# Kernel tuning notes

Hardware: AMD Instinct MI355X
Metric: run time of the kernel (lower is better)

The kernel has to match this reference:

```python
import jax, jax.numpy as jnp
import numpy as np

# ---- init_kwargs constants ----
OFFSET = 1.0
TAU = 10.0
HX, HY = 1.0, 1.0
B, C, NX0, NY0 = 8, 1, 384, 384
KMAX = 30          # forward() calls BiCGSTAB_GS(kmax=30)
EPS = 1e-9
# forward() transposes dims 2,3 and swaps nx,ny:
NX, NY = NY0, NX0


def sym_pad(x):
    # torchvision Pad(1, padding_mode='symmetric')
    return jnp.pad(x, ((0, 0), (0, 0), (1, 1), (1, 1)), mode='symmetric')


def zero_pad(x):
    return jnp.pad(x, ((0, 0), (0, 0), (1, 1), (1, 1)))


def zero_pad_gs(x):
    return zero_pad(x[:, :, 1:NX + 1, 1:NY + 1])


def fro(x):
    # Frobenius norm over spatial dims, NaN-safe at 0 for AD.
    sq = jnp.sum(x * x, axis=(2, 3))
    return jnp.where(sq > 0, jnp.sqrt(jnp.where(sq > 0, sq, 1.0)), 0.0)


def make_stencil(V, mask1, mask2):
    Vp = jnp.swapaxes(sym_pad(V), 2, 3) + OFFSET          # (B,C,NX+2,NY+2)
    m1 = jnp.swapaxes(sym_pad(mask1), 2, 3)
    m2 = jnp.swapaxes(sym_pad(mask2), 2, 3)
    # conv2d(V,f1)/conv2d(V,f2): forward-diff / pairwise average
    d1r = ((Vp[:, :, 1:, :] - Vp[:, :, :-1, :]) / HX) / (0.5 * (Vp[:, :, 1:, :] + Vp[:, :, :-1, :]))
    d2r = ((Vp[:, :, :, 1:] - Vp[:, :, :, :-1]) / HY) / (0.5 * (Vp[:, :, :, 1:] + Vp[:, :, :, :-1]))
    d1 = jnp.zeros((B, C, NX + 2, NY + 2), V.dtype).at[:, :, :NX + 1, 1:NY + 1].set(d1r[:, :, :, 1:NY + 1]) * m1
    d2 = jnp.zeros((B, C, NX + 2, NY + 2), V.dtype).at[:, :, 1:NX + 1, :NY + 1].set(d2r[:, :, 1:NX + 1, :]) * m2
    rx, ry = TAU / (2.0 * HX), TAU / (2.0 * HY)
    rxx, ryy = TAU / (HX * HX), TAU / (HY * HY)
    # conv 'same' with kernels [1,-1,0]: out[i] = d[i-1] - d[i] (zero beyond edge)
    dd1 = jnp.pad(d1, ((0, 0), (0, 0), (1, 0), (0, 0)))[:, :, :-1, :] - d1
    dd2 = jnp.pad(d2, ((0, 0), (0, 0), (0, 0), (1, 0)))[:, :, :, :-1] - d2
    boo = (1.0 + 2.0 * (rxx + ryy) - rx * dd1 - ry * dd2)[:, :, 1:NX + 1, 1:NY + 1]
    bpo = -rxx + rx * d1[:, :, 1:NX + 1, 1:NY + 1]
    bop = -ryy + ry * d2[:, :, 1:NX + 1, 1:NY + 1]
    bmo = -rxx - rx * d1[:, :, :NX, 1:NY + 1]
    bom = -ryy - ry * d2[:, :, 1:NX + 1, :NY]
    return boo, bmo, bom, bop, bpo


def apply_stencil(x, st):
    boo, bmo, bom, bop, bpo = st
    inp = sym_pad(x[:, :, 1:NX + 1, 1:NY + 1])
    res = (boo * inp[:, :, 1:NX + 1, 1:NY + 1]
           + bmo * inp[:, :, :NX, 1:NY + 1]
           + bom * inp[:, :, 1:NX + 1, :NY]
           + bop * inp[:, :, 1:NX + 1, 2:NY + 2]
           + bpo * inp[:, :, 2:NX + 2, 1:NY + 1])
    return zero_pad(res)


def bicgstab(x, b, st):
    thr = EPS * NX * NY
    r0 = apply_stencil(x, st)
    p = zero_pad_gs(b - r0)
    r_0, r = p, p
    r0_abs = fro(p)
    r_abs = r0_abs
    zs = jnp.zeros((B, C), x.dtype)
    k = jnp.zeros((B, C), jnp.int32)
    z4 = jnp.zeros_like(x)
    carry = (x, r_0, r, z4, p, z4, z4, z4, k, r_abs, zs, r0_abs, zs, zs, zs, zs)

    def step(c, _):
        x, r_0, r, r_old, p, v, s, t, k, r_abs, v_abs, r0_abs, sigma, alpha, omega, beta = c
        CONV = (k < KMAX) & (r_abs > thr)
        CONVe = CONV[:, :, None, None]
        v = jnp.where(CONVe, apply_stencil(p, st), v)
        sigma = jnp.where(CONV, jnp.sum(v * r_0, (2, 3)), sigma)
        v_abs = jnp.where(CONV, fro(v), v_abs)
        RES = sigma <= EPS * v_abs * r0_abs
        R1 = CONV & RES
        R1e = R1[:, :, None, None]
        p = jnp.where(R1e, zero_pad_gs(b - apply_stencil(x, st)), p)
        r = jnp.where(R1e, p, r)
        r_0 = jnp.where(R1e, p, r_0)
        r0_abs = jnp.where(R1, fro(r_0), r0_abs)
        r_abs = jnp.where(R1, r0_abs, r_abs)
        k = jnp.where(R1, k + 1, k)
        NR = CONV & ~RES
        NRe = NR[:, :, None, None]
        sig_safe = jnp.where(NR, sigma, 1.0)
        alpha = jnp.where(NR, jnp.sum(r * r_0, (2, 3)) / sig_safe, alpha)
        s = jnp.where(NRe, r - alpha[:, :, None, None] * v, s)
        C2 = fro(s) <= thr
        C3 = NR & C2
        C3e = C3[:, :, None, None]
        x = jnp.where(C3e, x + alpha[:, :, None, None] * p, x)
        r = jnp.where(C3e, s, r)
        C4 = NR & ~C2
        C4e = C4[:, :, None, None]
        t = jnp.where(C4e, apply_stencil(s, st), t)
        tt = jnp.where(C4, jnp.sum(t * t, (2, 3)), 1.0)
        omega = jnp.where(C4, jnp.sum(t * s, (2, 3)) / tt, omega)
        x = jnp.where(C4e, x + alpha[:, :, None, None] * p + omega[:, :, None, None] * s, x)
        r_old = jnp.where(C4e, r, r_old)
        r = jnp.where(C4e, s - omega[:, :, None, None] * t, r)
        om_safe = jnp.where(C4, omega, 1.0)
        den = jnp.where(C4, jnp.sum(r_old * r_0, (2, 3)), 1.0)
        beta = jnp.where(C4, alpha / om_safe * (jnp.sum(r * r_0, (2, 3)) / den), beta)
        p = jnp.where(C4e, r + beta[:, :, None, None] * (p - omega[:, :, None, None] * v), p)
        k = jnp.where(NR, k + 1, k)
        r_abs = jnp.where(NR, fro(r), r_abs)
        return (x, r_0, r, r_old, p, v, s, t, k, r_abs, v_abs, r0_abs, sigma, alpha, omega, beta), None

    carry, _ = jax.lax.scan(step, carry, None, length=KMAX)
    return carry[0]


def setup_inputs():
    key = jax.random.key(0)
    k1, k2, k3 = jax.random.split(key, 3)
    V = jax.random.uniform(k1, (B, C, NX0, NY0), jnp.float32)
    mask1 = jax.random.uniform(k2, (B, C, NX0, NY0), jnp.float32)
    mask2 = jax.random.uniform(k3, (B, C, NX0, NY0), jnp.float32)
    return {"V": V, "mask1": mask1, "mask2": mask2}


def reference(V, mask1, mask2):
    st = make_stencil(V, mask1, mask2)
    Um = jnp.mean(V, axis=(2, 3), keepdims=True) * jnp.ones_like(V)
    U = jnp.swapaxes(sym_pad(Um), 2, 3) + OFFSET
    x = bicgstab(U, U, st)   # BiCGSTAB_GS(x=U, b=U)
    return x[:, :, 1:-1, 1:-1]
```

## Files before the change

kernel.cpp:

```cpp
#include <hip/hip_runtime.h>

#define NXI 384
#define NG  (NXI*NXI)
#define NSYS 8
#define BPS 32
#define NBLK (NSYS*BPS)
#define NTHR 512
#define ROWS_PB 12
#define EPB (ROWS_PB*NXI)
#define EPT (EPB/NTHR)

#define THRC 1.47456e-4f

__device__ __forceinline__ float aloadf(const float* p) {
  return __hip_atomic_load(p, __ATOMIC_RELAXED, __HIP_MEMORY_SCOPE_AGENT);
}
__device__ __forceinline__ void astoref(float* p, float v) {
  __hip_atomic_store(p, v, __ATOMIC_RELAXED, __HIP_MEMORY_SCOPE_AGENT);
}
__device__ __forceinline__ double aloadd(const double* p) {
  return __hip_atomic_load(p, __ATOMIC_RELAXED, __HIP_MEMORY_SCOPE_AGENT);
}
__device__ __forceinline__ void astored(double* p, double v) {
  __hip_atomic_store(p, v, __ATOMIC_RELAXED, __HIP_MEMORY_SCOPE_AGENT);
}

__device__ __forceinline__ double wave_red(double v) {
#pragma unroll
  for (int off = 32; off > 0; off >>= 1) v += __shfl_down(v, off, 64);
  return v;
}

__device__ __forceinline__ void sys_bar(unsigned* flags, unsigned* phase, int tid, int bs) {
  __atomic_signal_fence(__ATOMIC_SEQ_CST);
  __builtin_amdgcn_s_waitcnt(0);
  __syncthreads();
  const unsigned ph = ++(*phase);
  if (tid == 0) {
    __hip_atomic_store(flags + bs, ph, __ATOMIC_RELAXED, __HIP_MEMORY_SCOPE_AGENT);
  }
  if (tid < 64) {
    while (true) {
      const unsigned f = __hip_atomic_load(flags + (tid & 31), __ATOMIC_RELAXED,
                                           __HIP_MEMORY_SCOPE_AGENT);
      if (__ballot(f >= ph) == ~0ull) break;
      __builtin_amdgcn_s_sleep(1);
    }
  }
  __syncthreads();
  __atomic_signal_fence(__ATOMIC_SEQ_CST);
}

__device__ __forceinline__ void bredN(const double* v, int n,
                                      double* slots, int chan0,
                                      int sys, int bs, int tid) {
  __shared__ double sred[NTHR/64][5];
  const int wid = tid >> 6, lane = tid & 63;
#pragma unroll
  for (int q = 0; q < n; q++) {
    const double w = wave_red(v[q]);
    if (lane == 0) sred[wid][q] = w;
  }
  __syncthreads();
  if (tid == 0) {
#pragma unroll
    for (int q = 0; q < n; q++) {
      double a = 0.0;
#pragma unroll
      for (int w2 = 0; w2 < NTHR/64; w2++) a += sred[w2][q];
      astored(slots + (size_t)(chan0 + q) * NBLK + sys * BPS + bs, a);
    }
  }
  __syncthreads();
}

__device__ __forceinline__ void shredN(const double* slots, int chan0, int n,
                                       int sys, int lane, double* out) {
  double v[5];
#pragma unroll
  for (int q = 0; q < n; q++)
    v[q] = aloadd(slots + (size_t)(chan0 + q) * NBLK + sys * BPS + (lane & 31));
#pragma unroll
  for (int q = 0; q < n; q++) {
    double x = v[q];
    x += __shfl_xor(x, 1, 64);
    x += __shfl_xor(x, 2, 64);
    x += __shfl_xor(x, 4, 64);
    x += __shfl_xor(x, 8, 64);
    x += __shfl_xor(x, 16, 64);
    out[q] = x;
  }
}

__device__ __forceinline__ float froguard(double sq) {
  return sq > 0.0 ? (float)sqrt(sq) : 0.0f;
}

__device__ __forceinline__ void coef5(const float* __restrict__ Vb,
                                      const float* __restrict__ M1b,
                                      const float* __restrict__ M2b,
                                      int i, int j, float* c5) {
  const int a0 = (i - 1 < 0) ? 0 : i - 1;
  const int a2 = (i + 1 > NXI - 1) ? NXI - 1 : i + 1;
  const int b0 = (j - 1 < 0) ? 0 : j - 1;
  const int b2 = (j + 1 > NXI - 1) ? NXI - 1 : j + 1;
  const float vc = Vb[j * NXI + i] + 1.0f;
  const float vu = Vb[j * NXI + a0] + 1.0f;
  const float vd = Vb[j * NXI + a2] + 1.0f;
  const float vl = Vb[b0 * NXI + i] + 1.0f;
  const float vr = Vb[b2 * NXI + i] + 1.0f;
  const float D1A = M1b[j * NXI + i] * ((vd - vc) / (0.5f * (vd + vc)));
  const float D1B = M1b[j * NXI + a0] * ((vc - vu) / (0.5f * (vc + vu)));
  const float D2A = M2b[j * NXI + i] * ((vr - vc) / (0.5f * (vr + vc)));
  const float D2B = M2b[b0 * NXI + i] * ((vc - vl) / (0.5f * (vc + vl)));
  c5[0] = 41.0f - 5.0f * (D1B - D1A) - 5.0f * (D2B - D2A);
  c5[1] = -10.0f - 5.0f * D1B;
  c5[2] = -10.0f - 5.0f * D2B;
  c5[3] = -10.0f + 5.0f * D2A;
  c5[4] = -10.0f + 5.0f * D1A;
}

__global__ __launch_bounds__(NTHR, 1) void bicg_kernel(
    const float* __restrict__ V, const float* __restrict__ M1, const float* __restrict__ M2,
    float* __restrict__ xout, float* __restrict__ wsf) {
  const int blk = blockIdx.x;
  const int sys = blk & (NSYS - 1);
  const int bs  = blk >> 3;
  const int tid = threadIdx.x;
  const int lane = tid & 63;
  const int gr0 = bs * ROWS_PB;

  __shared__ float slabP[14 * NXI];
  __shared__ float slabS[14 * NXI];
  __shared__ float vgh[2 * NXI];
  __shared__ float tgh[2 * NXI];
  __shared__ float rgh[2 * NXI];
  __shared__ float bcf[4];
  __shared__ int   bci[1];
  __shared__ float sh_r0abs, sh_rho;
  __shared__ double sh_ss2;

  unsigned* flags = (unsigned*)wsf + sys * 32;
  double* slots = (double*)(wsf + 1024);
  float* ghv_all = wsf + 16384;
  float* ght_all = ghv_all + (size_t)NSYS * BPS * 2 * NXI;
  float* ghx_all = ght_all + (size_t)NSYS * BPS * 2 * NXI;
  float* ghq_all = ghx_all + (size_t)NSYS * BPS * 2 * NXI;
  float* ghv = ghv_all + (size_t)sys * BPS * 2 * NXI;
  float* ght = ght_all + (size_t)sys * BPS * 2 * NXI;
  float* ghx = ghx_all + (size_t)sys * BPS * 2 * NXI;
  float* ghq = ghq_all + (size_t)sys * BPS * 2 * NXI;
  float* ghv_own = ghv + (size_t)bs * 2 * NXI;
  float* ght_own = ght + (size_t)bs * 2 * NXI;
  float* ghx_own = ghx + (size_t)bs * 2 * NXI;
  float* ghq_own = ghq + (size_t)bs * 2 * NXI;

  unsigned bphase = 0;

  const size_t so = (size_t)sys * NG;
  const float* Vb  = V  + so;
  const float* M1b = M1 + so;
  const float* M2b = M2 + so;
  float* xs = xout + so + (size_t)bs * EPB;

  float cboo_r[EPT], cbmo_r[EPT], cbom_r[EPT], cbop_r[EPT], cbpo_r[EPT];
#pragma unroll
  for (int k = 0; k < EPT; k++) {
    const int e = tid + k * NTHR;
    const int lr = e / NXI, c = e - lr * NXI;
    float c5[5];
    coef5(Vb, M1b, M2b, gr0 + lr, c, c5);
    cboo_r[k] = c5[0]; cbmo_r[k] = c5[1]; cbom_r[k] = c5[2];
    cbop_r[k] = c5[3]; cbpo_r[k] = c5[4];
  }
  {
    double vsum = 0.0;
#pragma unroll
    for (int k = 0; k < EPT; k++) vsum += (double)Vb[bs * EPB + tid + k * NTHR];
    bredN(&vsum, 1, slots, 9, sys, bs, tid);
  }
  sys_bar(flags, &bphase, tid, bs);

  double smb[1]; shredN(slots, 9, 1, sys, lane, smb);
  const float mb = (float)(smb[0] / (double)NG) + 1.0f;
  float preg[EPT], rreg[EPT], r0reg[EPT], vreg[EPT], treg[EPT], xreg[EPT];
#pragma unroll
  for (int k = 0; k < EPT; k++) {
    const int e = tid + k * NTHR;
    const int ce = e + NXI;
    const float ax = (cboo_r[k] + cbmo_r[k] + cbom_r[k] + cbop_r[k] + cbpo_r[k]) * mb;
    const float pn = mb - ax;
    xreg[k] = mb;
    preg[k] = pn; rreg[k] = pn; r0reg[k] = pn;
    slabP[ce] = pn;
  }
  for (int g = tid; g < 2 * NXI; g += NTHR) {
    const bool top = g < NXI;
    if (top ? (bs > 0) : (bs < BPS - 1)) {
      const int c = top ? g : g - NXI;
      const int ci = top ? c : 13 * NXI + c;
      const int gi = top ? gr0 - 1 : gr0 + ROWS_PB;
      float c5[5];
      coef5(Vb, M1b, M2b, gi, c, c5);
      const float pn = mb - (c5[0] + c5[1] + c5[2] + c5[3] + c5[4]) * mb;
      slabP[ci] = pn;
      rgh[g] = pn;
    }
  }
  if (tid == 0) { bcf[3] = 1.0f; bci[0] = 0; }

  for (int it = 0; it < 30; ++it) {
    __syncthreads();
    if (!(bcf[3] > THRC)) break;

    {
      double d[5] = {0, 0, 0, 0, 0};
#pragma unroll
      for (int k = 0; k < EPT; k++) {
        const int e = tid + k * NTHR;
        const int lr = e / NXI, c = e - lr * NXI;
        const int gr = gr0 + lr;
        const int ce = e + NXI;
        const float uc = preg[k];
        const float um = (gr == 0)       ? uc : slabP[ce - NXI];
        const float ud = (gr == NXI - 1) ? uc : slabP[ce + NXI];
        const float ul = (c == 0)        ? uc : slabP[ce - 1];
        const float ur = (c == NXI - 1)  ? uc : slabP[ce + 1];
        const float vv = cboo_r[k] * uc + cbmo_r[k] * um + cbom_r[k] * ul + cbop_r[k] * ur + cbpo_r[k] * ud;
        vreg[k] = vv;
        if (lr == 0)  astoref(ghv_own + c, vv);
        if (lr == 11) astoref(ghv_own + NXI + c, vv);
        d[0] += (double)vv * (double)r0reg[k];
        d[1] += (double)vv * (double)vv;
        d[2] += (double)rreg[k] * (double)r0reg[k];
        d[3] += (double)rreg[k] * (double)vv;
        d[4] += (double)rreg[k] * (double)rreg[k];
      }
      bredN(d, 5, slots, 0, sys, bs, tid);
    }
    sys_bar(flags, &bphase, tid, bs);

    if (tid < 64) {
      double s[5];
      shredN(slots, 0, 5, sys, lane, s);
      const float sigma = (float)s[0];
      const float v_abs = froguard(s[1]);
      const float rho_l = (float)s[2];
      const float r0a = (it == 0) ? froguard(s[4]) : sh_r0abs;
      int code = 0;
      float al = 0.f, ra = 0.f;
      double ss2 = 0.0;
      if (it == 0 && !(r0a > THRC)) {
        code = 3; ra = r0a;
      } else if (sigma <= 1e-9f * v_abs * r0a) {
        code = 1;
      } else {
        al = rho_l / sigma;
        const double da = (double)al;
        ss2 = s[4] - 2.0 * da * s[3] + da * da * s[1];
        const float s_abs = froguard(ss2);
        if (s_abs <= THRC) { code = 2; ra = s_abs; }
      }
      if (lane == 0) {
        bci[0] = code; bcf[0] = al;
        if (code == 2 || code == 3) bcf[3] = ra;
        sh_ss2 = ss2; sh_rho = rho_l;
        if (it == 0) sh_r0abs = r0a;
      }
    } else {
      for (int g = tid - 64; g < 2 * NXI; g += NTHR - 64) {
        const bool top = g < NXI;
        const int c = top ? g : g - NXI;
        if (top) { if (bs > 0)       vgh[g] = aloadf(ghv + (size_t)(bs - 1) * 2 * NXI + NXI + c); }
        else     { if (bs < BPS - 1) vgh[g] = aloadf(ghv + (size_t)(bs + 1) * 2 * NXI + c); }
      }
    }
    __syncthreads();
    const int code = bci[0];

    if (code == 3) continue;

    if (code == 1) {
#pragma unroll
      for (int k = 0; k < EPT; k++) {
        const int e = tid + k * NTHR;
        const int lr = e / NXI, c = e - lr * NXI;
        slabS[e + NXI] = xreg[k];
        if (lr == 0)  astoref(ghx_own + c, xreg[k]);
        if (lr == 11) astoref(ghx_own + NXI + c, xreg[k]);
      }
      sys_bar(flags, &bphase, tid, bs);
      for (int g = tid; g < 2 * NXI; g += NTHR) {
        const bool top = g < NXI;
        const int c = top ? g : g - NXI;
        if (top) { if (bs > 0)       slabS[c]            = aloadf(ghx + (size_t)(bs - 1) * 2 * NXI + NXI + c); }
        else     { if (bs < BPS - 1) slabS[13 * NXI + c] = aloadf(ghx + (size_t)(bs + 1) * 2 * NXI + c); }
      }
      __syncthreads();
#pragma unroll
      for (int k = 0; k < EPT; k++) {
        const int e = tid + k * NTHR;
        const int lr = e / NXI, c = e - lr * NXI;
        const int gr = gr0 + lr;
        const int ce = e + NXI;
        const float uc = xreg[k];
        const float um = (gr == 0)       ? uc : slabS[ce - NXI];
        const float ud = (gr == NXI - 1) ? uc : slabS[ce + NXI];
        const float ul = (c == 0)        ? uc : slabS[ce - 1];
        const float ur = (c == NXI - 1)  ? uc : slabS[ce + 1];
        treg[k] = mb - (cboo_r[k] * uc + cbmo_r[k] * um + cbom_r[k] * ul + cbop_r[k] * ur + cbpo_r[k] * ud);
      }
      __syncthreads();
      {
        double pp = 0;
#pragma unroll
        for (int k = 0; k < EPT; k++) {
          const int e = tid + k * NTHR;
          const int lr = e / NXI, c = e - lr * NXI;
          const float pn = treg[k];
          preg[k] = pn; rreg[k] = pn; r0reg[k] = pn;
          slabP[e + NXI] = pn;
          if (lr == 0)  astoref(ghq_own + c, pn);
          if (lr == 11) astoref(ghq_own + NXI + c, pn);
          pp += (double)pn * (double)pn;
        }
        bredN(&pp, 1, slots, 10, sys, bs, tid);
      }
      sys_bar(flags, &bphase, tid, bs);
      if (tid < 64) {
        double sp[1]; shredN(slots, 10, 1, sys, lane, sp);
        const float ra = froguard(sp[0]);
        if (lane == 0) { bcf[3] = ra; sh_r0abs = ra; }
      } else {
        for (int g = tid - 64; g < 2 * NXI; g += NTHR - 64) {
          const bool top = g < NXI;
          const int c = top ? g : g - NXI;
          const int ci = top ? c : 13 * NXI + c;
          if (top ? (bs > 0) : (bs < BPS - 1)) {
            const float pn = top ? aloadf(ghq + (size_t)(bs - 1) * 2 * NXI + NXI + c)
                                 : aloadf(ghq + (size_t)(bs + 1) * 2 * NXI + c);
            slabP[ci] = pn;
            rgh[g] = pn;
          }
        }
      }
      continue;
    }

    const float alpha = bcf[0];
    if (code == 2) {
#pragma unroll
      for (int k = 0; k < EPT; k++) {
        xreg[k] = xreg[k] + alpha * preg[k];
        rreg[k] = rreg[k] - alpha * vreg[k];
      }
      continue;
    }

#pragma unroll
    for (int k = 0; k < EPT; k++) {
      const int e = tid + k * NTHR;
      slabS[e + NXI] = rreg[k] - alpha * vreg[k];
    }
    for (int g = tid; g < 2 * NXI; g += NTHR) {
      const bool top = g < NXI;
      if (top ? (bs > 0) : (bs < BPS - 1)) {
        const int c = top ? g : g - NXI;
        const int ci = top ? c : 13 * NXI + c;
        slabS[ci] = rgh[g] - alpha * vgh[g];
      }
    }
    __syncthreads();
    {
      double d[4] = {0, 0, 0, 0};
#pragma unroll
      for (int k = 0; k < EPT; k++) {
        const int e = tid + k * NTHR;
        const int lr = e / NXI, c = e - lr * NXI;
        const int gr = gr0 + lr;
        const int ce = e + NXI;
        const float sc = rreg[k] - alpha * vreg[k];
        const float um = (gr == 0)       ? sc : slabS[ce - NXI];
        const float ud = (gr == NXI - 1) ? sc : slabS[ce + NXI];
        const float ul = (c == 0)        ? sc : slabS[ce - 1];
        const float ur = (c == NXI - 1)  ? sc : slabS[ce + 1];
        const float tv = cboo_r[k] * sc + cbmo_r[k] * um + cbom_r[k] * ul + cbop_r[k] * ur + cbpo_r[k] * ud;
        treg[k] = tv;
        if (lr == 0)  astoref(ght_own + c, tv);
        if (lr == 11) astoref(ght_own + NXI + c, tv);
        d[0] += (double)tv * (double)tv;
        d[1] += (double)tv * (double)sc;
        d[2] += (double)sc * (double)r0reg[k];
        d[3] += (double)tv * (double)r0reg[k];
      }
      bredN(d, 4, slots, 5, sys, bs, tid);
    }
    sys_bar(flags, &bphase, tid, bs);

    if (tid < 64) {
      double s2[4];
      shredN(slots, 5, 4, sys, lane, s2);
      const double tt = s2[0], ts = s2[1], sr0 = s2[2], tr0 = s2[3];
      const float om = (float)ts / (float)tt;
      const double dw = (double)om;
      const float rho_new = (float)(sr0 - dw * tr0);
      const double rr_new = sh_ss2 - 2.0 * dw * ts + dw * dw * tt;
      const float be = (bcf[0] / om) * (rho_new / sh_rho);
      if (lane == 0) {
        bcf[1] = om; bcf[2] = be; bcf[3] = froguard(rr_new);
      }
    } else {
      for (int g = tid - 64; g < 2 * NXI; g += NTHR - 64) {
        const bool top = g < NXI;
        const int c = top ? g : g - NXI;
        if (top) { if (bs > 0)       tgh[g] = aloadf(ght + (size_t)(bs - 1) * 2 * NXI + NXI + c); }
        else     { if (bs < BPS - 1) tgh[g] = aloadf(ght + (size_t)(bs + 1) * 2 * NXI + c); }
      }
    }
    __syncthreads();
    {
      const float omega = bcf[1];
      const float beta  = bcf[2];
#pragma unroll
      for (int k = 0; k < EPT; k++) {
        const int e = tid + k * NTHR;
        const float sc = rreg[k] - alpha * vreg[k];
        xreg[k] = xreg[k] + alpha * preg[k] + omega * sc;
        const float rn = sc - omega * treg[k];
        const float pn = rn + beta * (preg[k] - omega * vreg[k]);
        rreg[k] = rn;
        preg[k] = pn;
        slabP[e + NXI] = pn;
      }
      for (int g = tid; g < 2 * NXI; g += NTHR) {
        const bool top = g < NXI;
        if (top ? (bs > 0) : (bs < BPS - 1)) {
          const int c = top ? g : g - NXI;
          const int ci = top ? c : 13 * NXI + c;
          const float sg = slabS[ci];
          const float rg_new = sg - omega * tgh[g];
          const float pg_new = rg_new + beta * (slabP[ci] - omega * vgh[g]);
          rgh[g] = rg_new;
          slabP[ci] = pg_new;
        }
      }
    }
  }

#pragma unroll
  for (int k = 0; k < EPT; k++) {
    xs[tid + k * NTHR] = xreg[k];
  }
}

extern "C" void kernel_launch(void* const* d_in, const int* in_sizes, int n_in,
                              void* d_out, int out_size, void* d_ws, size_t ws_size,
                              hipStream_t stream) {
  const float* V  = (const float*)d_in[0];
  const float* M1 = (const float*)d_in[1];
  const float* M2 = (const float*)d_in[2];
  float* xout = (float*)d_out;
  float* wsf  = (float*)d_ws;
  hipMemsetAsync(d_ws, 0, 4096, stream);
  bicg_kernel<<<dim3(NBLK), dim3(NTHR), 0, stream>>>(V, M1, M2, xout, wsf);
}
```

Measured before the change: 461.6 us.

## Merge BiCGSTAB's two reductions per iteration into one via extra stencil products

Restructures each BiCGSTAB iteration so that only one grid-wide barrier and reduction is needed instead of two. The kernel computes v=A p, u=A r and w=A v up front, so t=A s can be formed as u - alpha*w. All fourteen inner products are then reduced together, and alpha, omega and beta come from a single combined result. To support this, each block keeps wider halos (two ghost rows for p and r, three for x) and exchanges v, u and w boundary rows. This trades an extra stencil application, more reduction channels and larger halo traffic for fewer cross-block synchronisations, and the recurrence-based dot products may drift slightly in float precision.

```diff
diff --git a/kernel.cpp b/kernel.cpp
--- a/kernel.cpp
+++ b/kernel.cpp
@@ -9,6 +9,8 @@
 #define ROWS_PB 12
 #define EPB (ROWS_PB*NXI)
 #define EPT (EPB/NTHR)
+#define SIDX(r) (((r)+2)*NXI)
+#define VIDX(r) (((r)+3)*NXI)
 
 #define THRC 1.47456e-4f
 
@@ -54,7 +56,7 @@
 __device__ __forceinline__ void bredN(const double* v, int n,
                                       double* slots, int chan0,
                                       int sys, int bs, int tid) {
-  __shared__ double sred[NTHR/64][5];
+  __shared__ double sred[NTHR/64][14];
   const int wid = tid >> 6, lane = tid & 63;
 #pragma unroll
   for (int q = 0; q < n; q++) {
@@ -76,7 +78,7 @@
 
 __device__ __forceinline__ void shredN(const double* slots, int chan0, int n,
                                        int sys, int lane, double* out) {
-  double v[5];
+  double v[14];
 #pragma unroll
   for (int q = 0; q < n; q++)
     v[q] = aloadd(slots + (size_t)(chan0 + q) * NBLK + sys * BPS + (lane & 31));
@@ -130,30 +132,25 @@
   const int lane = tid & 63;
   const int gr0 = bs * ROWS_PB;
 
-  __shared__ float slabP[14 * NXI];
-  __shared__ float slabS[14 * NXI];
-  __shared__ float vgh[2 * NXI];
-  __shared__ float tgh[2 * NXI];
-  __shared__ float rgh[2 * NXI];
+  __shared__ float slabP[16 * NXI];
+  __shared__ float slabR[16 * NXI];
+  __shared__ float slabV[18 * NXI];
+  __shared__ float cgh[2][5][NXI];
+  __shared__ float ghV[4 * NXI];
+  __shared__ float ghU[4 * NXI];
+  __shared__ float ghW[4 * NXI];
   __shared__ float bcf[4];
   __shared__ int   bci[1];
-  __shared__ float sh_r0abs, sh_rho;
-  __shared__ double sh_ss2;
+  __shared__ float sh_r0abs;
 
   unsigned* flags = (unsigned*)wsf + sys * 32;
   double* slots = (double*)(wsf + 1024);
-  float* ghv_all = wsf + 16384;
-  float* ght_all = ghv_all + (size_t)NSYS * BPS * 2 * NXI;
-  float* ghx_all = ght_all + (size_t)NSYS * BPS * 2 * NXI;
-  float* ghq_all = ghx_all + (size_t)NSYS * BPS * 2 * NXI;
-  float* ghv = ghv_all + (size_t)sys * BPS * 2 * NXI;
-  float* ght = ght_all + (size_t)sys * BPS * 2 * NXI;
-  float* ghx = ghx_all + (size_t)sys * BPS * 2 * NXI;
-  float* ghq = ghq_all + (size_t)sys * BPS * 2 * NXI;
-  float* ghv_own = ghv + (size_t)bs * 2 * NXI;
-  float* ght_own = ght + (size_t)bs * 2 * NXI;
-  float* ghx_own = ghx + (size_t)bs * 2 * NXI;
-  float* ghq_own = ghq + (size_t)bs * 2 * NXI;
+  float* ghp_all = wsf + 16384;
+  float* ghp_sys = ghp_all + (size_t)sys * (BPS * 12 * NXI);
+  float* ghp_own = ghp_sys + (size_t)bs * (12 * NXI);
+  float* ghx_all = ghp_all + (size_t)NSYS * BPS * 12 * NXI;
+  float* ghx_sys = ghx_all + (size_t)sys * (BPS * 6 * NXI);
+  float* ghx_own = ghx_sys + (size_t)bs * (6 * NXI);
 
   unsigned bphase = 0;
 
@@ -173,38 +170,48 @@
     cboo_r[k] = c5[0]; cbmo_r[k] = c5[1]; cbom_r[k] = c5[2];
     cbop_r[k] = c5[3]; cbpo_r[k] = c5[4];
   }
-  {
-    double vsum = 0.0;
-#pragma unroll
-    for (int k = 0; k < EPT; k++) vsum += (double)Vb[bs * EPB + tid + k * NTHR];
-    bredN(&vsum, 1, slots, 9, sys, bs, tid);
-  }
-  sys_bar(flags, &bphase, tid, bs);
-
-  double smb[1]; shredN(slots, 9, 1, sys, lane, smb);
-  const float mb = (float)(smb[0] / (double)NG) + 1.0f;
-  float preg[EPT], rreg[EPT], r0reg[EPT], vreg[EPT], treg[EPT], xreg[EPT];
-#pragma unroll
-  for (int k = 0; k < EPT; k++) {
-    const int e = tid + k * NTHR;
-    const int ce = e + NXI;
-    const float ax = (cboo_r[k] + cbmo_r[k] + cbom_r[k] + cbop_r[k] + cbpo_r[k]) * mb;
-    const float pn = mb - ax;
-    xreg[k] = mb;
-    preg[k] = pn; rreg[k] = pn; r0reg[k] = pn;
-    slabP[ce] = pn;
-  }
   for (int g = tid; g < 2 * NXI; g += NTHR) {
     const bool top = g < NXI;
     if (top ? (bs > 0) : (bs < BPS - 1)) {
       const int c = top ? g : g - NXI;
-      const int ci = top ? c : 13 * NXI + c;
+      const int side = top ? 0 : 1;
       const int gi = top ? gr0 - 1 : gr0 + ROWS_PB;
       float c5[5];
       coef5(Vb, M1b, M2b, gi, c, c5);
+      cgh[side][0][c] = c5[0]; cgh[side][1][c] = c5[1]; cgh[side][2][c] = c5[2];
+      cgh[side][3][c] = c5[3]; cgh[side][4][c] = c5[4];
+    }
+  }
+  {
+    double vsum = 0.0;
+#pragma unroll
+    for (int k = 0; k < EPT; k++) vsum += (double)Vb[bs * EPB + tid + k * NTHR];
+    bredN(&vsum, 1, slots, 14, sys, bs, tid);
+  }
+  sys_bar(flags, &bphase, tid, bs);
+
+  double smb[1]; shredN(slots, 14, 1, sys, lane, smb);
+  const float mb = (float)(smb[0] / (double)NG) + 1.0f;
+  float preg[EPT], rreg[EPT], r0reg[EPT], vreg[EPT], ureg[EPT], wreg[EPT], xreg[EPT];
+#pragma unroll
+  for (int k = 0; k < EPT; k++) {
+    const int e = tid + k * NTHR;
+    const int lr = e / NXI, c = e - lr * NXI;
+    const float pn = mb - (cboo_r[k] + cbmo_r[k] + cbom_r[k] + cbop_r[k] + cbpo_r[k]) * mb;
+    xreg[k] = mb;
+    preg[k] = pn; rreg[k] = pn; r0reg[k] = pn;
+    slabP[SIDX(lr) + c] = pn;
+    slabR[SIDX(lr) + c] = pn;
+  }
+  for (int g = tid; g < 4 * NXI; g += NTHR) {
+    const int slot = g / NXI, c = g - slot * NXI;
+    if (slot < 2 ? (bs > 0) : (bs < BPS - 1)) {
+      const int row = (slot == 0) ? -2 : (slot == 1) ? -1 : (slot == 2) ? ROWS_PB : ROWS_PB + 1;
+      float c5[5];
+      coef5(Vb, M1b, M2b, gr0 + row, c, c5);
       const float pn = mb - (c5[0] + c5[1] + c5[2] + c5[3] + c5[4]) * mb;
-      slabP[ci] = pn;
-      rgh[g] = pn;
+      slabP[SIDX(row) + c] = pn;
+      slabR[SIDX(row) + c] = pn;
     }
   }
   if (tid == 0) { bcf[3] = 1.0f; bci[0] = 0; }
@@ -213,66 +220,144 @@
     __syncthreads();
     if (!(bcf[3] > THRC)) break;
 
+#pragma unroll
+    for (int k = 0; k < EPT; k++) {
+      const int e = tid + k * NTHR;
+      const int lr = e / NXI, c = e - lr * NXI;
+      const int gr = gr0 + lr;
+      const float uc = preg[k];
+      const float um = (gr == 0)       ? uc : slabP[SIDX(lr - 1) + c];
+      const float ud = (gr == NXI - 1) ? uc : slabP[SIDX(lr + 1) + c];
+      const float ul = (c == 0)        ? uc : slabP[SIDX(lr) + c - 1];
+      const float ur = (c == NXI - 1)  ? uc : slabP[SIDX(lr) + c + 1];
+      const float vv = cboo_r[k] * uc + cbmo_r[k] * um + cbom_r[k] * ul + cbop_r[k] * ur + cbpo_r[k] * ud;
+      vreg[k] = vv;
+      slabV[VIDX(lr) + c] = vv;
+    }
+    for (int g = tid; g < 2 * NXI; g += NTHR) {
+      const bool top = g < NXI;
+      if (top ? (bs > 0) : (bs < BPS - 1)) {
+        const int c = top ? g : g - NXI;
+        const int row = top ? -1 : ROWS_PB;
+        const int side = top ? 0 : 1;
+        const float uc = slabP[SIDX(row) + c];
+        const float um = slabP[SIDX(row - 1) + c];
+        const float ud = slabP[SIDX(row + 1) + c];
+        const float ul = (c == 0)       ? uc : slabP[SIDX(row) + c - 1];
+        const float ur = (c == NXI - 1) ? uc : slabP[SIDX(row) + c + 1];
+        slabV[VIDX(row) + c] = cgh[side][0][c] * uc + cgh[side][1][c] * um +
+                               cgh[side][2][c] * ul + cgh[side][3][c] * ur + cgh[side][4][c] * ud;
+      }
+    }
+    __syncthreads();
+
     {
-      double d[5] = {0, 0, 0, 0, 0};
+      double d[14];
+#pragma unroll
+      for (int q = 0; q < 14; q++) d[q] = 0.0;
 #pragma unroll
       for (int k = 0; k < EPT; k++) {
         const int e = tid + k * NTHR;
         const int lr = e / NXI, c = e - lr * NXI;
         const int gr = gr0 + lr;
-        const int ce = e + NXI;
-        const float uc = preg[k];
-        const float um = (gr == 0)       ? uc : slabP[ce - NXI];
-        const float ud = (gr == NXI - 1) ? uc : slabP[ce + NXI];
-        const float ul = (c == 0)        ? uc : slabP[ce - 1];
-        const float ur = (c == NXI - 1)  ? uc : slabP[ce + 1];
-        const float vv = cboo_r[k] * uc + cbmo_r[k] * um + cbom_r[k] * ul + cbop_r[k] * ur + cbpo_r[k] * ud;
-        vreg[k] = vv;
-        if (lr == 0)  astoref(ghv_own + c, vv);
-        if (lr == 11) astoref(ghv_own + NXI + c, vv);
-        d[0] += (double)vv * (double)r0reg[k];
-        d[1] += (double)vv * (double)vv;
-        d[2] += (double)rreg[k] * (double)r0reg[k];
-        d[3] += (double)rreg[k] * (double)vv;
-        d[4] += (double)rreg[k] * (double)rreg[k];
-      }
-      bredN(d, 5, slots, 0, sys, bs, tid);
+        const float rc = rreg[k];
+        const float rum = (gr == 0)       ? rc : slabR[SIDX(lr - 1) + c];
+        const float rud = (gr == NXI - 1) ? rc : slabR[SIDX(lr + 1) + c];
+        const float rul = (c == 0)        ? rc : slabR[SIDX(lr) + c - 1];
+        const float rur = (c == NXI - 1)  ? rc : slabR[SIDX(lr) + c + 1];
+        const float uu_ = cboo_r[k] * rc + cbmo_r[k] * rum + cbom_r[k] * rul + cbop_r[k] * rur + cbpo_r[k] * rud;
+        ureg[k] = uu_;
+        const float vc = vreg[k];
+        const float vum = (gr == 0)       ? vc : slabV[VIDX(lr - 1) + c];
+        const float vud = (gr == NXI - 1) ? vc : slabV[VIDX(lr + 1) + c];
+        const float vul = (c == 0)        ? vc : slabV[VIDX(lr) + c - 1];
+        const float vur = (c == NXI - 1)  ? vc : slabV[VIDX(lr) + c + 1];
+        const float ww_ = cboo_r[k] * vc + cbmo_r[k] * vum + cbom_r[k] * vul + cbop_r[k] * vur + cbpo_r[k] * vud;
+        wreg[k] = ww_;
+        int slot = -1;
+        if (lr == 0) slot = 0; else if (lr == 1) slot = 1;
+        else if (lr == ROWS_PB - 2) slot = 2; else if (lr == ROWS_PB - 1) slot = 3;
+        if (slot >= 0) {
+          astoref(ghp_own + (0 * 4 + slot) * NXI + c, vc);
+          astoref(ghp_own + (1 * 4 + slot) * NXI + c, uu_);
+          astoref(ghp_own + (2 * 4 + slot) * NXI + c, ww_);
+        }
+        const double dv = vc, du = uu_, dww = ww_, dr = rc, dr0 = r0reg[k];
+        d[0]  += dv * dr0;
+        d[1]  += dv * dv;
+        d[2]  += dr * dr0;
+        d[3]  += dr * dv;
+        d[4]  += dr * dr;
+        d[5]  += du * du;
+        d[6]  += du * dww;
+        d[7]  += dww * dww;
+        d[8]  += du * dr;
+        d[9]  += du * dv;
+        d[10] += dww * dr;
+        d[11] += dww * dv;
+        d[12] += du * dr0;
+        d[13] += dww * dr0;
+      }
+      bredN(d, 14, slots, 0, sys, bs, tid);
     }
     sys_bar(flags, &bphase, tid, bs);
 
     if (tid < 64) {
-      double s[5];
-      shredN(slots, 0, 5, sys, lane, s);
+      double s[14];
+      shredN(slots, 0, 14, sys, lane, s);
       const float sigma = (float)s[0];
       const float v_abs = froguard(s[1]);
-      const float rho_l = (float)s[2];
+      const float rho_f = (float)s[2];
       const float r0a = (it == 0) ? froguard(s[4]) : sh_r0abs;
       int code = 0;
-      float al = 0.f, ra = 0.f;
-      double ss2 = 0.0;
+      float al = 0.f, om = 0.f, be = 0.f, ra = 0.f;
       if (it == 0 && !(r0a > THRC)) {
         code = 3; ra = r0a;
       } else if (sigma <= 1e-9f * v_abs * r0a) {
         code = 1;
       } else {
-        al = rho_l / sigma;
+        al = rho_f / sigma;
         const double da = (double)al;
-        ss2 = s[4] - 2.0 * da * s[3] + da * da * s[1];
+        const double ss2 = s[4] - 2.0 * da * s[3] + da * da * s[1];
         const float s_abs = froguard(ss2);
-        if (s_abs <= THRC) { code = 2; ra = s_abs; }
+        if (s_abs <= THRC) {
+          code = 2; ra = s_abs;
+        } else {
+          const double tt = s[5] - 2.0 * da * s[6] + da * da * s[7];
+          const double ts = s[8] - da * s[9] - da * s[10] + da * da * s[11];
+          om = (float)ts / (float)tt;
+          const double dwv = (double)om;
+          const double sr0 = s[2] - da * s[0];
+          const double tr0 = s[12] - da * s[13];
+          const float rho_new = (float)(sr0 - dwv * tr0);
+          be = (al / om) * (rho_new / rho_f);
+          const double rr_new = ss2 - 2.0 * dwv * ts + dwv * dwv * tt;
+          ra = froguard(rr_new);
+        }
       }
       if (lane == 0) {
-        bci[0] = code; bcf[0] = al;
-        if (code == 2 || code == 3) bcf[3] = ra;
-        sh_ss2 = ss2; sh_rho = rho_l;
+        bci[0] = code; bcf[0] = al; bcf[1] = om; bcf[2] = be;
+        if (code != 1) bcf[3] = ra;
         if (it == 0) sh_r0abs = r0a;
       }
     } else {
-      for (int g = tid - 64; g < 2 * NXI; g += NTHR - 64) {
-        const bool top = g < NXI;
-        const int c = top ? g : g - NXI;
-        if (top) { if (bs > 0)       vgh[g] = aloadf(ghv + (size_t)(bs - 1) * 2 * NXI + NXI + c); }
-        else     { if (bs < BPS - 1) vgh[g] = aloadf(ghv + (size_t)(bs + 1) * 2 * NXI + c); }
+      for (int g = tid - 64; g < 4 * NXI; g += NTHR - 64) {
+        const int slot = g / NXI, c = g - slot * NXI;
+        if (slot < 2) {
+          if (bs > 0) {
+            const float* src = ghp_sys + (size_t)(bs - 1) * (12 * NXI);
+            ghV[g] = aloadf(src + (0 * 4 + slot + 2) * NXI + c);
+            ghU[g] = aloadf(src + (1 * 4 + slot + 2) * NXI + c);
+            ghW[g] = aloadf(src + (2 * 4 + slot + 2) * NXI + c);
+          }
+        } else {
+          if (bs < BPS - 1) {
+            const float* src = ghp_sys + (size_t)(bs + 1) * (12 * NXI);
+            ghV[g] = aloadf(src + (0 * 4 + slot - 2) * NXI + c);
+            ghU[g] = aloadf(src + (1 * 4 + slot - 2) * NXI + c);
+            ghW[g] = aloadf(src + (2 * 4 + slot - 2) * NXI + c);
+          }
+        }
       }
     }
     __syncthreads();
@@ -285,163 +370,109 @@
       for (int k = 0; k < EPT; k++) {
         const int e = tid + k * NTHR;
         const int lr = e / NXI, c = e - lr * NXI;
-        slabS[e + NXI] = xreg[k];
-        if (lr == 0)  astoref(ghx_own + c, xreg[k]);
-        if (lr == 11) astoref(ghx_own + NXI + c, xreg[k]);
+        slabV[VIDX(lr) + c] = xreg[k];
+        if (lr <= 2)           astoref(ghx_own + lr * NXI + c, xreg[k]);
+        if (lr >= ROWS_PB - 3) astoref(ghx_own + (lr - (ROWS_PB - 3) + 3) * NXI + c, xreg[k]);
       }
       sys_bar(flags, &bphase, tid, bs);
-      for (int g = tid; g < 2 * NXI; g += NTHR) {
-        const bool top = g < NXI;
-        const int c = top ? g : g - NXI;
-        if (top) { if (bs > 0)       slabS[c]            = aloadf(ghx + (size_t)(bs - 1) * 2 * NXI + NXI + c); }
-        else     { if (bs < BPS - 1) slabS[13 * NXI + c] = aloadf(ghx + (size_t)(bs + 1) * 2 * NXI + c); }
+      for (int g = tid; g < 6 * NXI; g += NTHR) {
+        const int slot = g / NXI, c = g - slot * NXI;
+        if (slot < 3) {
+          if (bs > 0)
+            slabV[VIDX(slot - 3) + c] =
+                aloadf(ghx_sys + (size_t)(bs - 1) * (6 * NXI) + (slot + 3) * NXI + c);
+        } else {
+          if (bs < BPS - 1)
+            slabV[VIDX(ROWS_PB + slot - 3) + c] =
+                aloadf(ghx_sys + (size_t)(bs + 1) * (6 * NXI) + (slot - 3) * NXI + c);
+        }
       }
       __syncthreads();
+      {
+        double pp = 0.0;
+#pragma unroll
+        for (int k = 0; k < EPT; k++) {
+          const int e = tid + k * NTHR;
+          const int lr = e / NXI, c = e - lr * NXI;
+          const int gr = gr0 + lr;
+          const float uc = xreg[k];
+          const float um = (gr == 0)       ? uc : slabV[VIDX(lr - 1) + c];
+          const float ud = (gr == NXI - 1) ? uc : slabV[VIDX(lr + 1) + c];
+          const float ul = (c == 0)        ? uc : slabV[VIDX(lr) + c - 1];
+          const float ur = (c == NXI - 1)  ? uc : slabV[VIDX(lr) + c + 1];
+          const float pn = mb - (cboo_r[k] * uc + cbmo_r[k] * um + cbom_r[k] * ul + cbop_r[k] * ur + cbpo_r[k] * ud);
+          preg[k] = pn; rreg[k] = pn; r0reg[k] = pn;
+          slabP[SIDX(lr) + c] = pn;
+          slabR[SIDX(lr) + c] = pn;
+          pp += (double)pn * (double)pn;
+        }
+        for (int g = tid; g < 4 * NXI; g += NTHR) {
+          const int slot = g / NXI, c = g - slot * NXI;
+          if (slot < 2 ? (bs > 0) : (bs < BPS - 1)) {
+            const int row = (slot == 0) ? -2 : (slot == 1) ? -1 : (slot == 2) ? ROWS_PB : ROWS_PB + 1;
+            float c5[5];
+            coef5(Vb, M1b, M2b, gr0 + row, c, c5);
+            const float uc = slabV[VIDX(row) + c];
+            const float um = slabV[VIDX(row - 1) + c];
+            const float ud = slabV[VIDX(row + 1) + c];
+            const float ul = (c == 0)       ? uc : slabV[VIDX(row) + c - 1];
+            const float ur = (c == NXI - 1) ? uc : slabV[VIDX(row) + c + 1];
+            const float pn = mb - (c5[0] * uc + c5[1] * um + c5[2] * ul + c5[3] * ur + c5[4] * ud);
+            slabP[SIDX(row) + c] = pn;
+            slabR[SIDX(row) + c] = pn;
+          }
+        }
+        bredN(&pp, 1, slots, 15, sys, bs, tid);
+      }
+      sys_bar(flags, &bphase, tid, bs);
+      if (tid < 64) {
+        double sp[1]; shredN(slots, 15, 1, sys, lane, sp);
+        const float ra2 = froguard(sp[0]);
+        if (lane == 0) { bcf[3] = ra2; sh_r0abs = ra2; }
+      }
+      continue;
+    }
+
+    const float alpha = bcf[0];
+    if (code == 2) {
+#pragma unroll
+      for (int k = 0; k < EPT; k++) {
+        xreg[k] = xreg[k] + alpha * preg[k];
+        rreg[k] = rreg[k] - alpha * vreg[k];
+      }
+      continue;
+    }
+
+    {
+      const float omega = bcf[1];
+      const float beta  = bcf[2];
 #pragma unroll
       for (int k = 0; k < EPT; k++) {
         const int e = tid + k * NTHR;
         const int lr = e / NXI, c = e - lr * NXI;
-        const int gr = gr0 + lr;
-        const int ce = e + NXI;
-        const float uc = xreg[k];
-        const float um = (gr == 0)       ? uc : slabS[ce - NXI];
-        const float ud = (gr == NXI - 1) ? uc : slabS[ce + NXI];
-        const float ul = (c == 0)        ? uc : slabS[ce - 1];
-        const float ur = (c == NXI - 1)  ? uc : slabS[ce + 1];
-        treg[k] = mb - (cboo_r[k] * uc + cbmo_r[k] * um + cbom_r[k] * ul + cbop_r[k] * ur + cbpo_r[k] * ud);
-      }
-      __syncthreads();
-      {
-        double pp = 0;
-#pragma unroll
-        for (int k = 0; k < EPT; k++) {
-          const int e = tid + k * NTHR;
-          const int lr = e / NXI, c = e - lr * NXI;
-          const float pn = treg[k];
-          preg[k] = pn; rreg[k] = pn; r0reg[k] = pn;
-          slabP[e + NXI] = pn;
-          if (lr == 0)  astoref(ghq_own + c, pn);
-          if (lr == 11) astoref(ghq_own + NXI + c, pn);
-          pp += (double)pn * (double)pn;
-        }
-        bredN(&pp, 1, slots, 10, sys, bs, tid);
-      }
-      sys_bar(flags, &bphase, tid, bs);
-      if (tid < 64) {
-        double sp[1]; shredN(slots, 10, 1, sys, lane, sp);
-        const float ra = froguard(sp[0]);
-        if (lane == 0) { bcf[3] = ra; sh_r0abs = ra; }
-      } else {
-        for (int g = tid - 64; g < 2 * NXI; g += NTHR - 64) {
-          const bool top = g < NXI;
-          const int c = top ? g : g - NXI;
-          const int ci = top ? c : 13 * NXI + c;
-          if (top ? (bs > 0) : (bs < BPS - 1)) {
-            const float pn = top ? aloadf(ghq + (size_t)(bs - 1) * 2 * NXI + NXI + c)
-                                 : aloadf(ghq + (size_t)(bs + 1) * 2 * NXI + c);
-            slabP[ci] = pn;
-            rgh[g] = pn;
-          }
-        }
-      }
-      continue;
-    }
-
-    const float alpha = bcf[0];
-    if (code == 2) {
-#pragma unroll
-      for (int k = 0; k < EPT; k++) {
-        xreg[k] = xreg[k] + alpha * preg[k];
-        rreg[k] = rreg[k] - alpha * vreg[k];
-      }
-      continue;
-    }
-
-#pragma unroll
-    for (int k = 0; k < EPT; k++) {
-      const int e = tid + k * NTHR;
-      slabS[e + NXI] = rreg[k] - alpha * vreg[k];
-    }
-    for (int g = tid; g < 2 * NXI; g += NTHR) {
-      const bool top = g < NXI;
-      if (top ? (bs > 0) : (bs < BPS - 1)) {
-        const int c = top ? g : g - NXI;
-        const int ci = top ? c : 13 * NXI + c;
-        slabS[ci] = rgh[g] - alpha * vgh[g];
-      }
-    }
-    __syncthreads();
-    {
-      double d[4] = {0, 0, 0, 0};
-#pragma unroll
-      for (int k = 0; k < EPT; k++) {
-        const int e = tid + k * NTHR;
-        const int lr = e / NXI, c = e - lr * NXI;
-        const int gr = gr0 + lr;
-        const int ce = e + NXI;
         const float sc = rreg[k] - alpha * vreg[k];
-        const float um = (gr == 0)       ? sc : slabS[ce - NXI];
-        const float ud = (gr == NXI - 1) ? sc : slabS[ce + NXI];
-        const float ul = (c == 0)        ? sc : slabS[ce - 1];
-        const float ur = (c == NXI - 1)  ? sc : slabS[ce + 1];
-        const float tv = cboo_r[k] * sc + cbmo_r[k] * um + cbom_r[k] * ul + cbop_r[k] * ur + cbpo_r[k] * ud;
-        treg[k] = tv;
-        if (lr == 0)  astoref(ght_own + c, tv);
-        if (lr == 11) astoref(ght_own + NXI + c, tv);
-        d[0] += (double)tv * (double)tv;
-        d[1] += (double)tv * (double)sc;
-        d[2] += (double)sc * (double)r0reg[k];
-        d[3] += (double)tv * (double)r0reg[k];
-      }
-      bredN(d, 4, slots, 5, sys, bs, tid);
-    }
-    sys_bar(flags, &bphase, tid, bs);
-
-    if (tid < 64) {
-      double s2[4];
-      shredN(slots, 5, 4, sys, lane, s2);
-      const double tt = s2[0], ts = s2[1], sr0 = s2[2], tr0 = s2[3];
-      const float om = (float)ts / (float)tt;
-      const double dw = (double)om;
-      const float rho_new = (float)(sr0 - dw * tr0);
-      const double rr_new = sh_ss2 - 2.0 * dw * ts + dw * dw * tt;
-      const float be = (bcf[0] / om) * (rho_new / sh_rho);
-      if (lane == 0) {
-        bcf[1] = om; bcf[2] = be; bcf[3] = froguard(rr_new);
-      }
-    } else {
-      for (int g = tid - 64; g < 2 * NXI; g += NTHR - 64) {
-        const bool top = g < NXI;
-        const int c = top ? g : g - NXI;
-        if (top) { if (bs > 0)       tgh[g] = aloadf(ght + (size_t)(bs - 1) * 2 * NXI + NXI + c); }
-        else     { if (bs < BPS - 1) tgh[g] = aloadf(ght + (size_t)(bs + 1) * 2 * NXI + c); }
-      }
-    }
-    __syncthreads();
-    {
-      const float omega = bcf[1];
-      const float beta  = bcf[2];
-#pragma unroll
-      for (int k = 0; k < EPT; k++) {
-        const int e = tid + k * NTHR;
-        const float sc = rreg[k] - alpha * vreg[k];
+        const float tv = ureg[k] - alpha * wreg[k];
         xreg[k] = xreg[k] + alpha * preg[k] + omega * sc;
-        const float rn = sc - omega * treg[k];
+        const float rn = sc - omega * tv;
         const float pn = rn + beta * (preg[k] - omega * vreg[k]);
         rreg[k] = rn;
         preg[k] = pn;
-        slabP[e + NXI] = pn;
-      }
-      for (int g = tid; g < 2 * NXI; g += NTHR) {
-        const bool top = g < NXI;
-        if (top ? (bs > 0) : (bs < BPS - 1)) {
-          const int c = top ? g : g - NXI;
-          const int ci = top ? c : 13 * NXI + c;
-          const float sg = slabS[ci];
-          const float rg_new = sg - omega * tgh[g];
-          const float pg_new = rg_new + beta * (slabP[ci] - omega * vgh[g]);
-          rgh[g] = rg_new;
-          slabP[ci] = pg_new;
+        slabP[SIDX(lr) + c] = pn;
+        slabR[SIDX(lr) + c] = rn;
+      }
+      for (int g = tid; g < 4 * NXI; g += NTHR) {
+        const int slot = g / NXI, c = g - slot * NXI;
+        if (slot < 2 ? (bs > 0) : (bs < BPS - 1)) {
+          const int row = (slot == 0) ? -2 : (slot == 1) ? -1 : (slot == 2) ? ROWS_PB : ROWS_PB + 1;
+          const int si = SIDX(row) + c;
+          const float vg = ghV[g], ug = ghU[g], wg = ghW[g];
+          const float rold = slabR[si], pold = slabP[si];
+          const float sg = rold - alpha * vg;
+          const float tg = ug - alpha * wg;
+          const float rn = sg - omega * tg;
+          const float pn = rn + beta * (pold - omega * vg);
+          slabR[si] = rn;
+          slabP[si] = pn;
         }
       }
     }
```

Result: slower. 714.5 us (+54.8%).
